# Kernel tuning notes

Hardware: AMD Instinct MI355X
Metric: run time of the kernel (lower is better)

The kernel has to match this reference:

```python
import jax, jax.numpy as jnp
import numpy as np

B, N, DIM, H, DH, P = 4, 4096, 256, 8, 64, 2
INNER = H * DH  # 512


def setup_inputs() -> dict:
    key = jax.random.key(0)
    ks = jax.random.split(key, 10)
    w = lambda k, shape: jax.random.normal(k, shape, dtype=jnp.float32) * 0.02
    return dict(
        x=jax.random.normal(ks[0], (B, N, DIM), dtype=jnp.float32),
        prev_x=jax.random.normal(ks[1], (B, N, DIM), dtype=jnp.float32),
        ln_q_g=jnp.ones((2 * DIM,), jnp.float32), ln_q_b=jnp.zeros((2 * DIM,), jnp.float32),
        ln_k_g=jnp.ones((DIM,), jnp.float32), ln_k_b=jnp.zeros((DIM,), jnp.float32),
        ln_v_g=jnp.ones((DIM,), jnp.float32), ln_v_b=jnp.zeros((DIM,), jnp.float32),
        Wq=w(ks[2], (2 * DIM, INNER)),            # to_q, bias=False
        Wk=w(ks[3], (DIM, INNER)), bk=jnp.zeros((INNER,), jnp.float32),
        Wv=w(ks[4], (DIM, INNER)), bv=jnp.zeros((INNER,), jnp.float32),
        Woff=w(ks[5], (H * P, INNER)),            # 1x1 conv == linear over channels
        boff=jax.random.uniform(ks[6], (H * P,), jnp.float32, -1.0, 1.0),
        Wout=w(ks[7], (DIM, INNER)), bout=jnp.zeros((DIM,), jnp.float32),
    )


def _ln(x, g, b):
    m = x.mean(-1, keepdims=True)
    v = ((x - m) ** 2).mean(-1, keepdims=True)
    return (x - m) * jax.lax.rsqrt(v + 1e-5) * g + b


def reference(x, prev_x, ln_q_g, ln_q_b, ln_k_g, ln_k_b, ln_v_g, ln_v_b,
              Wq, Wk, bk, Wv, bv, Woff, boff, Wout, bout):
    scale = DH ** -0.5
    # queries from cat(x, prev_x) along feature dim
    q = _ln(jnp.concatenate([x, prev_x], axis=-1), ln_q_g, ln_q_b) @ Wq  # (B,N,INNER)
    # learned per-head, per-point offsets (1x1 conv over channels)
    offsets = (q @ Woff.T + boff).reshape(B, N, H, P).transpose(0, 2, 3, 1)  # (B,H,P,N)
    # K/V from cat(x, prev_x) along batch dim -> KV length 2N per (b,h)
    kv = jnp.concatenate([x, prev_x], axis=0)  # (2B,N,DIM)
    k = (_ln(kv, ln_k_g, ln_k_b) @ Wk + bk).reshape(2, B, N, H, DH).transpose(1, 3, 4, 0, 2).reshape(B, H, DH, 2 * N)
    v = (_ln(kv, ln_v_g, ln_v_b) @ Wv + bv).reshape(2, B, N, H, DH).transpose(1, 3, 4, 0, 2).reshape(B, H, DH, 2 * N)
    # sampling positions: pos + offset, clamped, truncated to int (matches torch .long())
    pos = jnp.arange(N, dtype=jnp.float32)
    samp = jnp.clip(pos[None, None, None, :] + offsets, 0, 2 * N - 1).astype(jnp.int32)  # (B,H,P,N)
    idx = samp.transpose(0, 1, 3, 2)[:, :, None, :, :]  # (B,H,1,N,P)
    k_s = jnp.take_along_axis(k[:, :, :, None, :], idx, axis=-1)  # (B,H,DH,N,P)
    v_s = jnp.take_along_axis(v[:, :, :, None, :], idx, axis=-1)  # (B,H,DH,N,P)
    qh = q.reshape(B, N, H, DH).transpose(0, 2, 1, 3) * scale     # (B,H,N,DH)
    sim = jnp.einsum('bhnd,bhdnp->bhnp', qh, k_s)                  # (B,H,N,P)
    attn = jax.nn.softmax(sim, axis=-1)
    out = jnp.einsum('bhnp,bhdnp->bhnd', attn, v_s)                # (B,H,N,DH)
    out = out.transpose(0, 2, 1, 3).reshape(B, N, INNER) @ Wout.T + bout  # (B,N,DIM)
    return out, offsets
```

## Files before the change

kernel.cpp:

```cpp
#include <hip/hip_runtime.h>
#include <hip/hip_bf16.h>
#include <math.h>

#define B_    4
#define N_    4096
#define DIM_  256
#define H_    8
#define DH_   64
#define P_    2
#define INNER_ 512
#define BN_   (B_ * N_)
#define KVR_  (2 * BN_)

typedef short v8s  __attribute__((ext_vector_type(8)));
typedef short v4s  __attribute__((ext_vector_type(4)));
typedef float v4f  __attribute__((ext_vector_type(4)));

__device__ __forceinline__ short f2b(float x) {
    __hip_bfloat16 h = __float2bfloat16(x);
    return *reinterpret_cast<short*>(&h);
}
__device__ __forceinline__ float b2f(short s) {
    __hip_bfloat16 h = *reinterpret_cast<__hip_bfloat16*>(&s);
    return __bfloat162float(h);
}

__device__ __forceinline__ void async16(const void* g, void* l) {
    __builtin_amdgcn_global_load_lds(
        (const __attribute__((address_space(1))) void*)g,
        (__attribute__((address_space(3))) void*)l, 16, 0, 0);
}

__device__ __forceinline__ void storeRow(float* p, float4 f0, float4 f1, float4 f2, float4 f3) {
    ((float4*)p)[0] = f0; ((float4*)p)[1] = f1; ((float4*)p)[2] = f2; ((float4*)p)[3] = f3;
}
__device__ __forceinline__ void storeRow(__hip_bfloat16* p, float4 f0, float4 f1, float4 f2, float4 f3) {
    v8s o0, o1;
    o0[0]=f2b(f0.x); o0[1]=f2b(f0.y); o0[2]=f2b(f0.z); o0[3]=f2b(f0.w);
    o0[4]=f2b(f1.x); o0[5]=f2b(f1.y); o0[6]=f2b(f1.z); o0[7]=f2b(f1.w);
    o1[0]=f2b(f2.x); o1[1]=f2b(f2.y); o1[2]=f2b(f2.z); o1[3]=f2b(f2.w);
    o1[4]=f2b(f3.x); o1[5]=f2b(f3.y); o1[6]=f2b(f3.z); o1[7]=f2b(f3.w);
    ((v8s*)p)[0] = o0; ((v8s*)p)[1] = o1;
}

__global__ void prep_t(const float* __restrict__ W, const float* __restrict__ g,
                       const float* __restrict__ beta, const float* __restrict__ bias_in,
                       short* __restrict__ Wt, float* __restrict__ b2, int K, int N) {
    int n = blockIdx.x, t = threadIdx.x;
    float partial = 0.f;
    for (int k = t; k < K; k += 256) {
        float w = W[k * N + n];
        Wt[(size_t)n * K + k] = f2b(g[k] * w);
        partial += beta[k] * w;
    }
    __shared__ float red[256];
    red[t] = partial;
    __syncthreads();
    for (int s = 128; s > 0; s >>= 1) {
        if (t < s) red[t] += red[t + s];
        __syncthreads();
    }
    if (t == 0) b2[n] = (bias_in ? bias_in[n] : 0.f) + red[0];
}

__global__ void cast_bf16(const float* __restrict__ src, short* __restrict__ dst, int n) {
    int i = blockIdx.x * 256 + threadIdx.x;
    if (i < n) dst[i] = f2b(src[i]);
}

__global__ void wcomb_kernel(const float* __restrict__ Wq, const float* __restrict__ gq,
                             const float* __restrict__ Woff, float* __restrict__ Wcomb) {
    int k = blockIdx.x, t = threadIdx.x;
    int hp = t & 15, jg = t >> 4;
    float p = 0.f;
    for (int j = jg; j < INNER_; j += 16)
        p += Wq[k * INNER_ + j] * Woff[hp * INNER_ + j];
    __shared__ float red[16][17];
    red[jg][hp] = p;
    __syncthreads();
    if (t < 16) {
        float s = 0.f;
        for (int i = 0; i < 16; i++) s += red[i][t];
        Wcomb[k * 16 + t] = gq[k] * s;
    }
}

__global__ void bcomb_kernel(const float* __restrict__ bq2, const float* __restrict__ Woff,
                             const float* __restrict__ boff, float* __restrict__ bcomb) {
    int t = threadIdx.x;
    int hp = t & 15, jg = t >> 4;
    float p = 0.f;
    for (int j = jg; j < INNER_; j += 16)
        p += bq2[j] * Woff[hp * INNER_ + j];
    __shared__ float red[16][17];
    red[jg][hp] = p;
    __syncthreads();
    if (t < 16) {
        float s = 0.f;
        for (int i = 0; i < 16; i++) s += red[i][t];
        bcomb[t] = s + boff[t];
    }
}

__global__ __launch_bounds__(256) void norm_fused_kernel(
    const float* __restrict__ x, const float* __restrict__ p,
    const float* __restrict__ Wcomb, const float* __restrict__ bcomb,
    short* __restrict__ Aq, short* __restrict__ Akv,
    float* __restrict__ out_off, int* __restrict__ idx) {
    const int lane = threadIdx.x & 63;
    const int wv   = threadIdx.x >> 6;
    const int m0   = (blockIdx.x * 4 + wv) * 4;
    const int k8   = lane * 8;

    float4 w[8][4];
#pragma unroll
    for (int i = 0; i < 8; i++) {
        const float4* wr = (const float4*)(Wcomb + (size_t)(k8 + i) * 16);
#pragma unroll
        for (int j = 0; j < 4; j++) w[i][j] = wr[j];
    }
    const float bc = bcomb[lane & 15];

    const float* srcb = (lane < 32) ? (x + k8) : (p + k8 - DIM_);

    float4 u0 = ((const float4*)(srcb + (size_t)m0 * DIM_))[0];
    float4 u1 = ((const float4*)(srcb + (size_t)m0 * DIM_))[1];

#pragma unroll
    for (int r = 0; r < 4; r++) {
        const int m = m0 + r;
        float4 n0, n1;
        if (r < 3) {
            n0 = ((const float4*)(srcb + (size_t)(m + 1) * DIM_))[0];
            n1 = ((const float4*)(srcb + (size_t)(m + 1) * DIM_))[1];
        }
        float uv[8] = { u0.x, u0.y, u0.z, u0.w, u1.x, u1.y, u1.z, u1.w };

        float s = 0.f, q2 = 0.f;
#pragma unroll
        for (int i = 0; i < 8; i++) { s += uv[i]; q2 += uv[i] * uv[i]; }
#pragma unroll
        for (int d = 1; d <= 16; d <<= 1) {
            s  += __shfl_xor(s, d);
            q2 += __shfl_xor(q2, d);
        }
        float mean_h = s * (1.f / 256.f);
        float var_h  = q2 * (1.f / 256.f) - mean_h * mean_h;
        float rstd_h = rsqrtf(var_h + 1e-5f);
        float sf  = s  + __shfl_xor(s, 32);
        float q2f = q2 + __shfl_xor(q2, 32);
        float mean_q = sf * (1.f / 512.f);
        float var_q  = q2f * (1.f / 512.f) - mean_q * mean_q;
        float rstd_q = rsqrtf(var_q + 1e-5f);

        v8s okv;
#pragma unroll
        for (int i = 0; i < 8; i++) okv[i] = f2b((uv[i] - mean_h) * rstd_h);
        short* akvdst = Akv + ((lane < 32) ? ((size_t)m * DIM_ + k8)
                                           : ((size_t)(BN_ + m) * DIM_ + k8 - DIM_));
        *(v8s*)akvdst = okv;

        float nv[8];
        v8s oq;
#pragma unroll
        for (int i = 0; i < 8; i++) { nv[i] = (uv[i] - mean_q) * rstd_q; oq[i] = f2b(nv[i]); }
        *(v8s*)(Aq + (size_t)m * INNER_ + k8) = oq;

        float acc[16];
#pragma unroll
        for (int h = 0; h < 16; h++) acc[h] = 0.f;
#pragma unroll
        for (int i = 0; i < 8; i++) {
            float nvi = nv[i];
            acc[0]  += nvi * w[i][0].x;  acc[1]  += nvi * w[i][0].y;
            acc[2]  += nvi * w[i][0].z;  acc[3]  += nvi * w[i][0].w;
            acc[4]  += nvi * w[i][1].x;  acc[5]  += nvi * w[i][1].y;
            acc[6]  += nvi * w[i][1].z;  acc[7]  += nvi * w[i][1].w;
            acc[8]  += nvi * w[i][2].x;  acc[9]  += nvi * w[i][2].y;
            acc[10] += nvi * w[i][2].z;  acc[11] += nvi * w[i][2].w;
            acc[12] += nvi * w[i][3].x;  acc[13] += nvi * w[i][3].y;
            acc[14] += nvi * w[i][3].z;  acc[15] += nvi * w[i][3].w;
        }
        float a8[8];
#pragma unroll
        for (int j = 0; j < 8; j++) {
            float lo = acc[2 * j] + __shfl_xor(acc[2 * j], 1);
            float hi = acc[2 * j + 1] + __shfl_xor(acc[2 * j + 1], 1);
            a8[j] = (lane & 1) ? hi : lo;
        }
        float a4[4];
#pragma unroll
        for (int j = 0; j < 4; j++) {
            float lo = a8[2 * j] + __shfl_xor(a8[2 * j], 2);
            float hi = a8[2 * j + 1] + __shfl_xor(a8[2 * j + 1], 2);
            a4[j] = (lane & 2) ? hi : lo;
        }
        float a2[2];
#pragma unroll
        for (int j = 0; j < 2; j++) {
            float lo = a4[2 * j] + __shfl_xor(a4[2 * j], 4);
            float hi = a4[2 * j + 1] + __shfl_xor(a4[2 * j + 1], 4);
            a2[j] = (lane & 4) ? hi : lo;
        }
        float l1 = a2[0] + __shfl_xor(a2[0], 8);
        float h1 = a2[1] + __shfl_xor(a2[1], 8);
        float a1 = (lane & 8) ? h1 : l1;
        a1 += __shfl_xor(a1, 16);
        a1 += __shfl_xor(a1, 32);

        if (lane < 16) {
            float off = a1 + bc;
            int b = m >> 12, n = m & (N_ - 1);
            int h = lane >> 1, pp = lane & 1;
            out_off[(size_t)((b * H_ + h) * P_ + pp) * N_ + n] = off;
            float f = fminf(fmaxf((float)n + off, 0.f), (float)(2 * N_ - 1));
            idx[((size_t)(b * H_ + h) * N_ + n) * P_ + pp] = (int)f;
        }
        u0 = n0; u1 = n1;
    }
}

template <typename OT>
__global__ __launch_bounds__(256) void gemm_mfma(
    const short* __restrict__ A, const short* __restrict__ Bt,
    const float* __restrict__ bias, OT* __restrict__ C, int M, int N, int K) {
    __shared__ short smem[2 * 128 * 64];
    short* As = smem;
    short* Bs = smem + 128 * 64;
    const int tid  = threadIdx.x;
    const int lane = tid & 63, w = tid >> 6;
    const int wr = w >> 1, wc = w & 1;
    const int lm = lane & 15, g = lane >> 4;

    const int nx  = gridDim.x;
    const int lin = blockIdx.y * nx + blockIdx.x;
    const int x8 = lin & 7, t = lin >> 3;
    const int bx = t % nx, by = (t / nx) * 8 + x8;
    const int row0 = by * 128, col0 = bx * 128;

    v4f acc[4][4];
#pragma unroll
    for (int i = 0; i < 4; i++)
#pragma unroll
        for (int j = 0; j < 4; j++) acc[i][j] = (v4f){0.f, 0.f, 0.f, 0.f};

    for (int k0 = 0; k0 < K; k0 += 64) {
        __syncthreads();
#pragma unroll
        for (int r = 0; r < 4; r++) {
            int s   = tid + 256 * r;
            int row = s >> 3, kcs = s & 7;
            int kg  = kcs ^ (row & 7);
            async16(A  + (size_t)(row0 + row) * K + k0 + kg * 8, (char*)As + s * 16);
            async16(Bt + (size_t)(col0 + row) * K + k0 + kg * 8, (char*)Bs + s * 16);
        }
        __syncthreads();
#pragma unroll
        for (int ks = 0; ks < 2; ks++) {
            v8s af[4], bf[4];
#pragma unroll
            for (int i = 0; i < 4; i++) {
                int m   = wr * 64 + i * 16 + lm;
                int sch = m * 8 + ((ks * 4 + g) ^ (m & 7));
                af[i] = *(const v8s*)(As + sch * 8);
            }
#pragma unroll
            for (int j = 0; j < 4; j++) {
                int n   = wc * 64 + j * 16 + lm;
                int sch = n * 8 + ((ks * 4 + g) ^ (n & 7));
                bf[j] = *(const v8s*)(Bs + sch * 8);
            }
#pragma unroll
            for (int i = 0; i < 4; i++)
#pragma unroll
                for (int j = 0; j < 4; j++)
                    acc[i][j] = __builtin_amdgcn_mfma_f32_16x16x32_bf16(af[i], bf[j], acc[i][j], 0, 0, 0);
        }
    }

#pragma unroll
    for (int j = 0; j < 4; j++) {
        int gc = col0 + wc * 64 + j * 16 + lm;
        float bj = bias ? bias[gc] : 0.f;
#pragma unroll
        for (int i = 0; i < 4; i++)
#pragma unroll
            for (int r = 0; r < 4; r++) acc[i][j][r] += bj;
    }

    __syncthreads();
    float* ep = (float*)smem + w * (16 * 68);
#pragma unroll
    for (int i = 0; i < 4; i++) {
#pragma unroll
        for (int j = 0; j < 4; j++)
#pragma unroll
            for (int r = 0; r < 4; r++)
                ep[(g * 4 + r) * 68 + j * 16 + lm] = acc[i][j][r];
        __syncthreads();
        int rr = lane >> 2, cb = (lane & 3) * 16;
        float4 f0 = *(float4*)(ep + rr * 68 + cb + 0);
        float4 f1 = *(float4*)(ep + rr * 68 + cb + 4);
        float4 f2 = *(float4*)(ep + rr * 68 + cb + 8);
        float4 f3 = *(float4*)(ep + rr * 68 + cb + 12);
        __syncthreads();
        int grow = row0 + wr * 64 + i * 16 + rr;
        int gcol = col0 + wc * 64 + cb;
        storeRow(&C[(size_t)grow * N + gcol], f0, f1, f2, f3);
    }
}

__global__ __launch_bounds__(256) void attn_kernel(
    const short* __restrict__ qb, const short* __restrict__ kvproj,
    const int* __restrict__ idx, short* __restrict__ attnout) {
    int lane = threadIdx.x & 63;
    int wv   = threadIdx.x >> 6;
    int n0 = blockIdx.x * 8 + wv * 2;
    int h = blockIdx.y, b = blockIdx.z;
    int mA = b * N_ + n0, mB = mA + 1;

    float qA = b2f(qb[(size_t)mA * INNER_ + h * DH_ + lane]) * 0.125f;
    float qB = b2f(qb[(size_t)mB * INNER_ + h * DH_ + lane]) * 0.125f;

    const int* ipA = idx + ((size_t)(b * H_ + h) * N_ + n0) * P_;
    int jA0 = ipA[0], jA1 = ipA[1], jB0 = ipA[2], jB1 = ipA[3];
    int rA0 = b * N_ + jA0 + ((jA0 >= N_) ? (BN_ - N_) : 0);
    int rA1 = b * N_ + jA1 + ((jA1 >= N_) ? (BN_ - N_) : 0);
    int rB0 = b * N_ + jB0 + ((jB0 >= N_) ? (BN_ - N_) : 0);
    int rB1 = b * N_ + jB1 + ((jB1 >= N_) ? (BN_ - N_) : 0);
    size_t oA0 = (size_t)rA0 * 1024 + h * DH_ + lane;
    size_t oA1 = (size_t)rA1 * 1024 + h * DH_ + lane;
    size_t oB0 = (size_t)rB0 * 1024 + h * DH_ + lane;
    size_t oB1 = (size_t)rB1 * 1024 + h * DH_ + lane;

    float kA0 = b2f(kvproj[oA0]),       kA1 = b2f(kvproj[oA1]);
    float kB0 = b2f(kvproj[oB0]),       kB1 = b2f(kvproj[oB1]);
    float vA0 = b2f(kvproj[oA0 + 512]), vA1 = b2f(kvproj[oA1 + 512]);
    float vB0 = b2f(kvproj[oB0 + 512]), vB1 = b2f(kvproj[oB1 + 512]);

    float sA0 = qA * kA0, sA1 = qA * kA1;
    float sB0 = qB * kB0, sB1 = qB * kB1;
    for (int d = 1; d < 64; d <<= 1) {
        sA0 += __shfl_xor(sA0, d);
        sA1 += __shfl_xor(sA1, d);
        sB0 += __shfl_xor(sB0, d);
        sB1 += __shfl_xor(sB1, d);
    }
    float mxA = fmaxf(sA0, sA1), mxB = fmaxf(sB0, sB1);
    float eA0 = __expf(sA0 - mxA), eA1 = __expf(sA1 - mxA);
    float eB0 = __expf(sB0 - mxB), eB1 = __expf(sB1 - mxB);
    float invA = 1.f / (eA0 + eA1), invB = 1.f / (eB0 + eB1);
    attnout[(size_t)mA * INNER_ + h * DH_ + lane] = f2b((eA0 * vA0 + eA1 * vA1) * invA);
    attnout[(size_t)mB * INNER_ + h * DH_ + lane] = f2b((eB0 * vB0 + eB1 * vB1) * invB);
}

extern "C" void kernel_launch(void* const* d_in, const int* in_sizes, int n_in,
                              void* d_out, int out_size, void* d_ws, size_t ws_size,
                              hipStream_t stream) {
    (void)in_sizes; (void)n_in; (void)out_size; (void)ws_size;

    const float* x      = (const float*)d_in[0];
    const float* prevx  = (const float*)d_in[1];
    const float* ln_q_g = (const float*)d_in[2];
    const float* ln_q_b = (const float*)d_in[3];
    const float* ln_k_g = (const float*)d_in[4];
    const float* ln_k_b = (const float*)d_in[5];
    const float* ln_v_g = (const float*)d_in[6];
    const float* ln_v_b = (const float*)d_in[7];
    const float* Wq     = (const float*)d_in[8];
    const float* Wk     = (const float*)d_in[9];
    const float* bk     = (const float*)d_in[10];
    const float* Wv     = (const float*)d_in[11];
    const float* bv     = (const float*)d_in[12];
    const float* Woff   = (const float*)d_in[13];
    const float* boff   = (const float*)d_in[14];
    const float* Wout   = (const float*)d_in[15];
    const float* bout   = (const float*)d_in[16];

    char* cur = (char*)d_ws;
    auto alloc = [&](size_t bytes) { char* p = cur; cur += (bytes + 255) & ~(size_t)255; return p; };
    short* Aq      = (short*)alloc((size_t)BN_ * INNER_ * 2);
    short* Akv     = (short*)alloc((size_t)KVR_ * DIM_ * 2);
    short* qb      = (short*)alloc((size_t)BN_ * INNER_ * 2);
    short* kvproj  = (short*)alloc((size_t)KVR_ * 1024 * 2);
    short* attnout = (short*)alloc((size_t)BN_ * INNER_ * 2);
    short* Wq2t    = (short*)alloc(512 * 512 * 2);
    short* Wkvt    = (short*)alloc(1024 * 256 * 2);
    short* Woutb   = (short*)alloc(256 * 512 * 2);
    float* bq2     = (float*)alloc(512 * 4);
    float* bkv     = (float*)alloc(1024 * 4);
    float* Wcomb   = (float*)alloc(512 * 16 * 4);
    float* bcomb   = (float*)alloc(16 * 4);
    int*   idxb    = (int*)alloc((size_t)BN_ * 16 * 4);

    float* out_main = (float*)d_out;
    float* out_off  = out_main + (size_t)BN_ * DIM_;

    prep_t<<<512, 256, 0, stream>>>(Wq, ln_q_g, ln_q_b, nullptr, Wq2t, bq2, 512, 512);
    prep_t<<<512, 256, 0, stream>>>(Wk, ln_k_g, ln_k_b, bk, Wkvt, bkv, 256, 512);
    prep_t<<<512, 256, 0, stream>>>(Wv, ln_v_g, ln_v_b, bv, Wkvt + 512 * 256, bkv + 512, 256, 512);
    cast_bf16<<<512, 256, 0, stream>>>(Wout, Woutb, 256 * 512);
    wcomb_kernel<<<512, 256, 0, stream>>>(Wq, ln_q_g, Woff, Wcomb);
    bcomb_kernel<<<1, 256, 0, stream>>>(bq2, Woff, boff, bcomb);

    norm_fused_kernel<<<BN_ / 16, 256, 0, stream>>>(x, prevx, Wcomb, bcomb,
                                                    Aq, Akv, out_off, idxb);

    gemm_mfma<__hip_bfloat16><<<dim3(INNER_ / 128, BN_ / 128), 256, 0, stream>>>(
        Aq, Wq2t, bq2, (__hip_bfloat16*)qb, BN_, INNER_, 512);
    gemm_mfma<__hip_bfloat16><<<dim3(1024 / 128, KVR_ / 128), 256, 0, stream>>>(
        Akv, Wkvt, bkv, (__hip_bfloat16*)kvproj, KVR_, 1024, 256);

    dim3 ga(N_ / 8, H_, B_);
    attn_kernel<<<ga, 256, 0, stream>>>(qb, kvproj, idxb, attnout);

    gemm_mfma<float><<<dim3(DIM_ / 128, BN_ / 128), 256, 0, stream>>>(
        attnout, Woutb, bout, out_main, BN_, DIM_, 512);
}
```

Baseline: 246.4 us.

## Merge prep kernels and QKV GEMMs, fold scale into Wq, vectorize attention

Combines the six weight-prep kernels into one prep_all launch plus a small bias-sum kernel, and merges the Q and KV GEMMs into a single launch that dispatches on block id. The 1/8 attention scale is folded into the prepped Wq and its bias. The attention kernel now has each 16-lane group handle one query with 4-wide bf16 vector loads, so the shuffle reduction is shorter and there are fewer scalar loads. The intent is to cut launch overhead and tail effects and to improve memory access efficiency in attention. The risk is that bf16 rounding of the pre-scaled Wq changes numerics slightly.

```diff
diff --git a/kernel.cpp b/kernel.cpp
--- a/kernel.cpp
+++ b/kernel.cpp
@@ -43,61 +43,73 @@
     ((v8s*)p)[0] = o0; ((v8s*)p)[1] = o1;
 }
 
-__global__ void prep_t(const float* __restrict__ W, const float* __restrict__ g,
-                       const float* __restrict__ beta, const float* __restrict__ bias_in,
-                       short* __restrict__ Wt, float* __restrict__ b2, int K, int N) {
-    int n = blockIdx.x, t = threadIdx.x;
-    float partial = 0.f;
-    for (int k = t; k < K; k += 256) {
-        float w = W[k * N + n];
-        Wt[(size_t)n * K + k] = f2b(g[k] * w);
-        partial += beta[k] * w;
-    }
-    __shared__ float red[256];
-    red[t] = partial;
-    __syncthreads();
-    for (int s = 128; s > 0; s >>= 1) {
-        if (t < s) red[t] += red[t + s];
-        __syncthreads();
-    }
-    if (t == 0) b2[n] = (bias_in ? bias_in[n] : 0.f) + red[0];
-}
-
-__global__ void cast_bf16(const float* __restrict__ src, short* __restrict__ dst, int n) {
-    int i = blockIdx.x * 256 + threadIdx.x;
-    if (i < n) dst[i] = f2b(src[i]);
-}
-
-__global__ void wcomb_kernel(const float* __restrict__ Wq, const float* __restrict__ gq,
-                             const float* __restrict__ Woff, float* __restrict__ Wcomb) {
-    int k = blockIdx.x, t = threadIdx.x;
-    int hp = t & 15, jg = t >> 4;
+__global__ __launch_bounds__(256) void prep_all(
+    const float* __restrict__ Wq, const float* __restrict__ gq, const float* __restrict__ betaq,
+    const float* __restrict__ Wk, const float* __restrict__ gk, const float* __restrict__ betak,
+    const float* __restrict__ bk,
+    const float* __restrict__ Wv, const float* __restrict__ gv, const float* __restrict__ betav,
+    const float* __restrict__ bv,
+    const float* __restrict__ Woff, const float* __restrict__ Wout,
+    short* __restrict__ Wq2t, float* __restrict__ bq2,
+    short* __restrict__ Wkvt, float* __restrict__ bkv,
+    float* __restrict__ Wcomb, float* __restrict__ braw, short* __restrict__ Woutb) {
+    __shared__ float sm[272];
+    const int bid = blockIdx.x, t = threadIdx.x;
+
+    if (bid < 1536) {
+        const float *W, *g, *beta, *bias_in;
+        short* Wt; float* b2; int K, n; float scale;
+        if (bid < 512)       { W=Wq; g=gq; beta=betaq; bias_in=nullptr; Wt=Wq2t; b2=bq2; K=512; n=bid;        scale=0.125f; }
+        else if (bid < 1024) { W=Wk; g=gk; beta=betak; bias_in=bk; Wt=Wkvt;           b2=bkv;       K=256; n=bid-512;  scale=1.f; }
+        else                 { W=Wv; g=gv; beta=betav; bias_in=bv; Wt=Wkvt+512*256;   b2=bkv+512;   K=256; n=bid-1024; scale=1.f; }
+        float partial = 0.f;
+        for (int k = t; k < K; k += 256) {
+            float w = W[k * 512 + n];
+            Wt[(size_t)n * K + k] = f2b(scale * g[k] * w);
+            partial += beta[k] * w;
+        }
+        sm[t] = partial;
+        __syncthreads();
+        for (int s = 128; s > 0; s >>= 1) {
+            if (t < s) sm[t] += sm[t + s];
+            __syncthreads();
+        }
+        if (t == 0) b2[n] = scale * ((bias_in ? bias_in[n] : 0.f) + sm[0]);
+    } else if (bid < 2048) {
+        const int k = bid - 1536;
+        const int hp = t & 15, jg = t >> 4;
+        float p = 0.f;
+        for (int j = jg; j < INNER_; j += 16)
+            p += Wq[k * INNER_ + j] * Woff[hp * INNER_ + j];
+        sm[jg * 17 + hp] = p;
+        __syncthreads();
+        if (t < 16) {
+            float s = 0.f;
+            for (int i = 0; i < 16; i++) s += sm[i * 17 + t];
+            Wcomb[k * 16 + t] = gq[k] * s;
+            braw[k * 16 + t]  = betaq[k] * s;
+        }
+    } else {
+        const int i0 = (bid - 2048) * 1024 + t * 4;
+        float4 f = *(const float4*)(Wout + i0);
+        v4s o;
+        o[0] = f2b(f.x); o[1] = f2b(f.y); o[2] = f2b(f.z); o[3] = f2b(f.w);
+        *(v4s*)(Woutb + i0) = o;
+    }
+}
+
+__global__ void bcomb_sum(const float* __restrict__ braw, const float* __restrict__ boff,
+                          float* __restrict__ bcomb) {
+    __shared__ float sm[272];
+    int t = threadIdx.x;
+    int hp = t & 15, kg = t >> 4;
     float p = 0.f;
-    for (int j = jg; j < INNER_; j += 16)
-        p += Wq[k * INNER_ + j] * Woff[hp * INNER_ + j];
-    __shared__ float red[16][17];
-    red[jg][hp] = p;
+    for (int k = kg; k < 512; k += 16) p += braw[k * 16 + hp];
+    sm[kg * 17 + hp] = p;
     __syncthreads();
     if (t < 16) {
         float s = 0.f;
-        for (int i = 0; i < 16; i++) s += red[i][t];
-        Wcomb[k * 16 + t] = gq[k] * s;
-    }
-}
-
-__global__ void bcomb_kernel(const float* __restrict__ bq2, const float* __restrict__ Woff,
-                             const float* __restrict__ boff, float* __restrict__ bcomb) {
-    int t = threadIdx.x;
-    int hp = t & 15, jg = t >> 4;
-    float p = 0.f;
-    for (int j = jg; j < INNER_; j += 16)
-        p += bq2[j] * Woff[hp * INNER_ + j];
-    __shared__ float red[16][17];
-    red[jg][hp] = p;
-    __syncthreads();
-    if (t < 16) {
-        float s = 0.f;
-        for (int i = 0; i < 16; i++) s += red[i][t];
+        for (int i = 0; i < 16; i++) s += sm[i * 17 + t];
         bcomb[t] = s + boff[t];
     }
 }
@@ -221,10 +233,9 @@
 }
 
 template <typename OT>
-__global__ __launch_bounds__(256) void gemm_mfma(
-    const short* __restrict__ A, const short* __restrict__ Bt,
-    const float* __restrict__ bias, OT* __restrict__ C, int M, int N, int K) {
-    __shared__ short smem[2 * 128 * 64];
+__device__ __forceinline__ void gemm_body(
+    short* smem, const short* __restrict__ A, const short* __restrict__ Bt,
+    const float* __restrict__ bias, OT* __restrict__ C, int N, int K, int nx, int lin) {
     short* As = smem;
     short* Bs = smem + 128 * 64;
     const int tid  = threadIdx.x;
@@ -232,8 +243,6 @@
     const int wr = w >> 1, wc = w & 1;
     const int lm = lane & 15, g = lane >> 4;
 
-    const int nx  = gridDim.x;
-    const int lin = blockIdx.y * nx + blockIdx.x;
     const int x8 = lin & 7, t = lin >> 3;
     const int bx = t % nx, by = (t / nx) * 8 + x8;
     const int row0 = by * 128, col0 = bx * 128;
@@ -310,48 +319,64 @@
     }
 }
 
+__global__ __launch_bounds__(256) void gemm_qkv(
+    const short* __restrict__ Aq, const short* __restrict__ Wq2t,
+    const float* __restrict__ bq2, __hip_bfloat16* __restrict__ qb,
+    const short* __restrict__ Akv, const short* __restrict__ Wkvt,
+    const float* __restrict__ bkv, __hip_bfloat16* __restrict__ kvproj) {
+    __shared__ short smem[2 * 128 * 64];
+    const int bid = blockIdx.x;
+    if (bid < 512)
+        gemm_body<__hip_bfloat16>(smem, Aq, Wq2t, bq2, qb, 512, 512, 4, bid);
+    else
+        gemm_body<__hip_bfloat16>(smem, Akv, Wkvt, bkv, kvproj, 1024, 256, 8, bid - 512);
+}
+
+__global__ __launch_bounds__(256) void gemm_out(
+    const short* __restrict__ A, const short* __restrict__ Bt,
+    const float* __restrict__ bias, float* __restrict__ C) {
+    __shared__ short smem[2 * 128 * 64];
+    const int lin = blockIdx.y * gridDim.x + blockIdx.x;
+    gemm_body<float>(smem, A, Bt, bias, C, 256, 512, 2, lin);
+}
+
 __global__ __launch_bounds__(256) void attn_kernel(
     const short* __restrict__ qb, const short* __restrict__ kvproj,
     const int* __restrict__ idx, short* __restrict__ attnout) {
-    int lane = threadIdx.x & 63;
-    int wv   = threadIdx.x >> 6;
-    int n0 = blockIdx.x * 8 + wv * 2;
-    int h = blockIdx.y, b = blockIdx.z;
-    int mA = b * N_ + n0, mB = mA + 1;
-
-    float qA = b2f(qb[(size_t)mA * INNER_ + h * DH_ + lane]) * 0.125f;
-    float qB = b2f(qb[(size_t)mB * INNER_ + h * DH_ + lane]) * 0.125f;
-
-    const int* ipA = idx + ((size_t)(b * H_ + h) * N_ + n0) * P_;
-    int jA0 = ipA[0], jA1 = ipA[1], jB0 = ipA[2], jB1 = ipA[3];
-    int rA0 = b * N_ + jA0 + ((jA0 >= N_) ? (BN_ - N_) : 0);
-    int rA1 = b * N_ + jA1 + ((jA1 >= N_) ? (BN_ - N_) : 0);
-    int rB0 = b * N_ + jB0 + ((jB0 >= N_) ? (BN_ - N_) : 0);
-    int rB1 = b * N_ + jB1 + ((jB1 >= N_) ? (BN_ - N_) : 0);
-    size_t oA0 = (size_t)rA0 * 1024 + h * DH_ + lane;
-    size_t oA1 = (size_t)rA1 * 1024 + h * DH_ + lane;
-    size_t oB0 = (size_t)rB0 * 1024 + h * DH_ + lane;
-    size_t oB1 = (size_t)rB1 * 1024 + h * DH_ + lane;
-
-    float kA0 = b2f(kvproj[oA0]),       kA1 = b2f(kvproj[oA1]);
-    float kB0 = b2f(kvproj[oB0]),       kB1 = b2f(kvproj[oB1]);
-    float vA0 = b2f(kvproj[oA0 + 512]), vA1 = b2f(kvproj[oA1 + 512]);
-    float vB0 = b2f(kvproj[oB0 + 512]), vB1 = b2f(kvproj[oB1 + 512]);
-
-    float sA0 = qA * kA0, sA1 = qA * kA1;
-    float sB0 = qB * kB0, sB1 = qB * kB1;
-    for (int d = 1; d < 64; d <<= 1) {
-        sA0 += __shfl_xor(sA0, d);
-        sA1 += __shfl_xor(sA1, d);
-        sB0 += __shfl_xor(sB0, d);
-        sB1 += __shfl_xor(sB1, d);
-    }
-    float mxA = fmaxf(sA0, sA1), mxB = fmaxf(sB0, sB1);
-    float eA0 = __expf(sA0 - mxA), eA1 = __expf(sA1 - mxA);
-    float eB0 = __expf(sB0 - mxB), eB1 = __expf(sB1 - mxB);
-    float invA = 1.f / (eA0 + eA1), invB = 1.f / (eB0 + eB1);
-    attnout[(size_t)mA * INNER_ + h * DH_ + lane] = f2b((eA0 * vA0 + eA1 * vA1) * invA);
-    attnout[(size_t)mB * INNER_ + h * DH_ + lane] = f2b((eB0 * vB0 + eB1 * vB1) * invB);
+    const int lane = threadIdx.x & 63;
+    const int wv   = threadIdx.x >> 6;
+    const int s    = lane >> 4, c = lane & 15;
+    const int n = blockIdx.x * 16 + wv * 4 + s;
+    const int h = blockIdx.y, b = blockIdx.z;
+    const int m = b * N_ + n;
+
+    v4s qv = *(const v4s*)(qb + (size_t)m * INNER_ + h * DH_ + c * 4);
+
+    const int* ip = idx + ((size_t)(b * H_ + h) * N_ + n) * P_;
+    int j0 = ip[0], j1 = ip[1];
+    int r0 = b * N_ + j0 + ((j0 >= N_) ? (BN_ - N_) : 0);
+    int r1 = b * N_ + j1 + ((j1 >= N_) ? (BN_ - N_) : 0);
+    const short* k0p = kvproj + (size_t)r0 * 1024 + h * DH_ + c * 4;
+    const short* k1p = kvproj + (size_t)r1 * 1024 + h * DH_ + c * 4;
+    v4s k0 = *(const v4s*)k0p, v0 = *(const v4s*)(k0p + 512);
+    v4s k1 = *(const v4s*)k1p, v1 = *(const v4s*)(k1p + 512);
+
+    float q0 = b2f(qv[0]), q1 = b2f(qv[1]), q2 = b2f(qv[2]), q3 = b2f(qv[3]);
+    float s0 = q0 * b2f(k0[0]) + q1 * b2f(k0[1]) + q2 * b2f(k0[2]) + q3 * b2f(k0[3]);
+    float s1 = q0 * b2f(k1[0]) + q1 * b2f(k1[1]) + q2 * b2f(k1[2]) + q3 * b2f(k1[3]);
+#pragma unroll
+    for (int d = 1; d <= 8; d <<= 1) {
+        s0 += __shfl_xor(s0, d);
+        s1 += __shfl_xor(s1, d);
+    }
+    float mx = fmaxf(s0, s1);
+    float e0 = __expf(s0 - mx), e1 = __expf(s1 - mx);
+    float inv = 1.f / (e0 + e1);
+    v4s o;
+#pragma unroll
+    for (int i = 0; i < 4; i++)
+        o[i] = f2b((e0 * b2f(v0[i]) + e1 * b2f(v1[i])) * inv);
+    *(v4s*)(attnout + (size_t)m * INNER_ + h * DH_ + c * 4) = o;
 }
 
 extern "C" void kernel_launch(void* const* d_in, const int* in_sizes, int n_in,
@@ -390,30 +415,28 @@
     float* bq2     = (float*)alloc(512 * 4);
     float* bkv     = (float*)alloc(1024 * 4);
     float* Wcomb   = (float*)alloc(512 * 16 * 4);
+    float* braw    = (float*)alloc(512 * 16 * 4);
     float* bcomb   = (float*)alloc(16 * 4);
     int*   idxb    = (int*)alloc((size_t)BN_ * 16 * 4);
 
     float* out_main = (float*)d_out;
     float* out_off  = out_main + (size_t)BN_ * DIM_;
 
-    prep_t<<<512, 256, 0, stream>>>(Wq, ln_q_g, ln_q_b, nullptr, Wq2t, bq2, 512, 512);
-    prep_t<<<512, 256, 0, stream>>>(Wk, ln_k_g, ln_k_b, bk, Wkvt, bkv, 256, 512);
-    prep_t<<<512, 256, 0, stream>>>(Wv, ln_v_g, ln_v_b, bv, Wkvt + 512 * 256, bkv + 512, 256, 512);
-    cast_bf16<<<512, 256, 0, stream>>>(Wout, Woutb, 256 * 512);
-    wcomb_kernel<<<512, 256, 0, stream>>>(Wq, ln_q_g, Woff, Wcomb);
-    bcomb_kernel<<<1, 256, 0, stream>>>(bq2, Woff, boff, bcomb);
+    prep_all<<<2176, 256, 0, stream>>>(Wq, ln_q_g, ln_q_b,
+                                       Wk, ln_k_g, ln_k_b, bk,
+                                       Wv, ln_v_g, ln_v_b, bv,
+                                       Woff, Wout,
+                                       Wq2t, bq2, Wkvt, bkv, Wcomb, braw, Woutb);
+    bcomb_sum<<<1, 256, 0, stream>>>(braw, boff, bcomb);
 
     norm_fused_kernel<<<BN_ / 16, 256, 0, stream>>>(x, prevx, Wcomb, bcomb,
                                                     Aq, Akv, out_off, idxb);
 
-    gemm_mfma<__hip_bfloat16><<<dim3(INNER_ / 128, BN_ / 128), 256, 0, stream>>>(
-        Aq, Wq2t, bq2, (__hip_bfloat16*)qb, BN_, INNER_, 512);
-    gemm_mfma<__hip_bfloat16><<<dim3(1024 / 128, KVR_ / 128), 256, 0, stream>>>(
-        Akv, Wkvt, bkv, (__hip_bfloat16*)kvproj, KVR_, 1024, 256);
-
-    dim3 ga(N_ / 8, H_, B_);
+    gemm_qkv<<<2560, 256, 0, stream>>>(Aq, Wq2t, bq2, (__hip_bfloat16*)qb,
+                                       Akv, Wkvt, bkv, (__hip_bfloat16*)kvproj);
+
+    dim3 ga(N_ / 16, H_, B_);
     attn_kernel<<<ga, 256, 0, stream>>>(qb, kvproj, idxb, attnout);
 
-    gemm_mfma<float><<<dim3(DIM_ / 128, BN_ / 128), 256, 0, stream>>>(
-        attnout, Woutb, bout, out_main, BN_, DIM_, 512);
-}
+    gemm_out<<<dim3(2, 128), 256, 0, stream>>>(attnout, Woutb, bout, out_main);
+}
```

After: 224.0 us. 9.1% less time.
